# Performance work log

Hardware: AMD Instinct MI355X
Metric: run time of the kernel (lower is better)

## Reference

```python
import jax, jax.numpy as jnp
import numpy as np
import math

D_MODEL = 512
N_HEADS = 2
B, S = 2, 1024
THRESHOLD = 0.5  # kwargs default 'sparsity_threshold'


def setup_inputs() -> dict:
    key = jax.random.key(0)
    ks = jax.random.split(key, 10)
    D, H = D_MODEL, D_MODEL // 4
    std = 0.02
    return {
        "x": jax.random.normal(ks[0], (B, S, D), jnp.float32),
        "Wq": jax.random.normal(ks[1], (D, D), jnp.float32) * std,
        "Wk": jax.random.normal(ks[2], (D, D), jnp.float32) * std,
        "Wv": jax.random.normal(ks[3], (D, D), jnp.float32) * std,
        "Wo": jax.random.normal(ks[4], (D, D), jnp.float32) * std,
        "bo": jnp.zeros((D,), jnp.float32),
        "W1": jax.random.normal(ks[5], (D, H), jnp.float32) * std,
        "b1": jnp.zeros((H,), jnp.float32),
        "W2": jax.random.normal(ks[6], (H, 1), jnp.float32) * std,
        "b2": jnp.zeros((1,), jnp.float32),
    }


def reference(x, Wq, Wk, Wv, Wo, bo, W1, b1, W2, b2):
    Bsz, Seq, D = x.shape
    Hn = N_HEADS
    dh = D // Hn

    def split_heads(t):
        return t.reshape(Bsz, Seq, Hn, dh).transpose(0, 2, 1, 3)  # [B,H,S,dh]

    q = split_heads(x @ Wq)
    k = split_heads(x @ Wk)
    v = split_heads(x @ Wv)

    scores = jnp.einsum("bhid,bhjd->bhij", q, k) / math.sqrt(dh)  # [B,H,S,S]

    # head-mean features for the pairwise sparsity predictor (n_heads==2 => 2*dh == D)
    q_mean = q.mean(axis=1)  # [B,S,dh]
    k_mean = k.mean(axis=1)  # [B,S,dh]
    # Linear1 of cat([q_mean_i, k_mean_j]) splits into two halves of W1
    a = q_mean @ W1[:dh]   # [B,S,Dh4]
    c = k_mean @ W1[dh:]   # [B,S,Dh4]
    hidden = jax.nn.relu(a[:, :, None, :] + c[:, None, :, :] + b1)  # [B,S,S,Dh4]
    connection_probs = jax.nn.sigmoid(jnp.squeeze(hidden @ W2, -1) + b2[0])  # [B,S,S]

    mask = connection_probs > THRESHOLD  # [B,S,S]
    scores = jnp.where(mask[:, None, :, :], scores, jnp.float32(-1e9))
    attn = jax.nn.softmax(scores, axis=-1)  # dropout inactive in eval

    out = jnp.einsum("bhij,bhjd->bhid", attn, v)  # [B,H,S,dh]
    out = out.transpose(0, 2, 1, 3).reshape(Bsz, Seq, D)
    out = out @ Wo + bo
    return out
```

## Files before the change

### kernel.cpp

```cpp
#include <hip/hip_runtime.h>


typedef unsigned short u16t;
typedef __bf16 bf16x8 __attribute__((ext_vector_type(8)));
typedef float f32x4 __attribute__((ext_vector_type(4)));

#define B_SZ 2
#define S_SZ 1024
#define D_SZ 512
#define DH 256
#define HH 128

static __device__ __forceinline__ u16t f2b(float f) {
    unsigned int u = __builtin_bit_cast(unsigned int, f);
    u += 0x7FFFu + ((u >> 16) & 1u);
    return (u16t)(u >> 16);
}

static __device__ __forceinline__ f32x4 mfma16(bf16x8 a, bf16x8 b, f32x4 c) {
    return __builtin_amdgcn_mfma_f32_16x16x32_bf16(a, b, c, 0, 0, 0);
}

static __device__ __forceinline__ void gload16(const void* g, void* l) {
    __builtin_amdgcn_global_load_lds(
        (const __attribute__((address_space(1))) void*)g,
        (__attribute__((address_space(3))) void*)l, 16, 0, 0);
}

__global__ __launch_bounds__(256) void k_prep(
    const float* __restrict__ x,
    const float* __restrict__ Wq, const float* __restrict__ Wk,
    const float* __restrict__ Wv, const float* __restrict__ Wo,
    const float* __restrict__ W1,
    u16t* __restrict__ xb, u16t* __restrict__ WT, float* __restrict__ Beff)
{
    __shared__ float smf[1088];
    int bidx = blockIdx.x;
    int t = threadIdx.x;
    if (bidx < 1024) {
        int idx = (bidx * 256 + t) * 4;
        float4 v = *(const float4*)(x + idx);
        u16t* o = xb + idx;
        o[0] = f2b(v.x); o[1] = f2b(v.y); o[2] = f2b(v.z); o[3] = f2b(v.w);
    } else if (bidx < 2048) {
        int t2 = bidx - 1024;
        int z = t2 >> 8, rem = t2 & 255;
        int n0 = (rem & 15) * 32, k0 = (rem >> 4) * 32;
        const float* W = z == 0 ? Wq : z == 1 ? Wk : z == 2 ? Wv : Wo;
        u16t* WTz = WT + (size_t)z * D_SZ * D_SZ;
        float (*tile)[33] = (float(*)[33])smf;
        int r = t >> 3, c4 = (t & 7) * 4;
        float4 v = *(const float4*)(W + (size_t)(k0 + r) * D_SZ + n0 + c4);
        tile[r][c4] = v.x; tile[r][c4 + 1] = v.y; tile[r][c4 + 2] = v.z; tile[r][c4 + 3] = v.w;
        __syncthreads();
        u16t o[4];
        o[0] = f2b(tile[c4][r]); o[1] = f2b(tile[c4 + 1][r]);
        o[2] = f2b(tile[c4 + 2][r]); o[3] = f2b(tile[c4 + 3][r]);
        *(ushort4*)(WTz + (size_t)(n0 + r) * D_SZ + k0 + c4) = *(ushort4*)o;
    } else {
        int k = bidx - 2048;
        float* wm0 = smf;
        float* wm1 = smf + 256;
        const float* wrq = Wq + (size_t)k * D_SZ;
        const float* wrk = Wk + (size_t)k * D_SZ;
        wm0[t & 255] = 0.5f * (wrq[t & 255] + wrq[(t & 255) + DH]);
        wm1[t & 255] = 0.5f * (wrk[t & 255] + wrk[(t & 255) + DH]);
        __syncthreads();
        int half = t >> 7, hcol = t & 127;
        const float* wm = half ? wm1 : wm0;
        const float* W1h = W1 + (half ? (size_t)DH * HH : 0);
        float s = 0.f;
        for (int d = 0; d < 256; ++d) s += wm[d] * W1h[(size_t)d * HH + hcol];
        Beff[(size_t)k * 256 + half * 128 + hcol] = s;
    }
}

template<int NF>
static __device__ __forceinline__ void gemm_mainloop(
    const u16t* __restrict__ A, int lda, const u16t* __restrict__ B, int ldb,
    int K, int tid, u16t* Als, u16t* Bls, f32x4 acc[2][NF])
{
    const int w = tid >> 6, lane = tid & 63;
    const int lr = lane & 15, kg = lane >> 4;
    const int srow = lane >> 3, scol = (lane & 7) * 8;
    for (int k0 = 0; k0 < K; k0 += 64) {
        if (k0) __syncthreads();
#pragma unroll
        for (int q = 0; q < 4; ++q) {
            int ci = w * 4 + q;
            gload16(A + (size_t)(ci * 8 + srow) * lda + k0 + scol, Als + ci * 512);
        }
#pragma unroll
        for (int q = 0; q < NF / 2; ++q) {
            int cj = w * (NF / 2) + q;
            gload16(B + (size_t)(cj * 8 + srow) * ldb + k0 + scol, Bls + cj * 512);
        }
        __syncthreads();
#pragma unroll
        for (int kk = 0; kk < 2; ++kk) {
            bf16x8 af[2], bfr[NF];
#pragma unroll
            for (int fi = 0; fi < 2; ++fi)
                af[fi] = *(const bf16x8*)(&Als[(w * 32 + fi * 16 + lr) * 64 + kk * 32 + kg * 8]);
#pragma unroll
            for (int fj = 0; fj < NF; ++fj)
                bfr[fj] = *(const bf16x8*)(&Bls[(fj * 16 + lr) * 64 + kk * 32 + kg * 8]);
#pragma unroll
            for (int fi = 0; fi < 2; ++fi)
#pragma unroll
                for (int fj = 0; fj < NF; ++fj)
                    acc[fi][fj] = mfma16(af[fi], bfr[fj], acc[fi][fj]);
        }
    }
}


__global__ __launch_bounds__(256) void k_qkvac(
    const u16t* __restrict__ xb, const u16t* __restrict__ WT,
    const float* __restrict__ x, const float* __restrict__ Beff,
    const float* __restrict__ b1,
    u16t* __restrict__ qb, u16t* __restrict__ kb, u16t* __restrict__ vT,
    float* __restrict__ a, float* __restrict__ cc)
{
    __shared__ __align__(16) char sm[27648];
    int bid = blockIdx.x;
    int t = threadIdx.x;
    if (bid < 384) {
        u16t* Als = (u16t*)sm;
        u16t* Bls = Als + 8192;
        int z = bid / 128, rem = bid & 127;
        int m0 = (rem >> 3) * 128, n0 = (rem & 7) * 64;
        const u16t* A = xb + (size_t)m0 * D_SZ;
        const u16t* Bt = WT + (size_t)z * D_SZ * D_SZ + (size_t)n0 * D_SZ;
        f32x4 acc[2][4] = {};
        gemm_mainloop<4>(A, D_SZ, Bt, D_SZ, D_SZ, t, Als, Bls, acc);
        int w = t >> 6, lane = t & 63, lr = lane & 15, kg = lane >> 4;
        __syncthreads();
        if (z < 2) {
            u16t (*vls)[68] = (u16t(*)[68])sm;
            float scale = z == 0 ? 0.0625f : 1.0f;
#pragma unroll
            for (int fi = 0; fi < 2; ++fi)
#pragma unroll
                for (int fj = 0; fj < 4; ++fj)
#pragma unroll
                    for (int rr = 0; rr < 4; ++rr)
                        vls[w * 32 + fi * 16 + kg * 4 + rr][fj * 16 + lr]
                            = f2b(acc[fi][fj][rr] * scale);
            __syncthreads();
            u16t* dst = z == 0 ? qb : kb;
            int c8 = (t & 7) * 8, r0 = t >> 3;
#pragma unroll
            for (int p = 0; p < 4; ++p) {
                int r = r0 + p * 32;
                *(uint4*)(dst + (size_t)(m0 + r) * D_SZ + n0 + c8) = *(const uint4*)(&vls[r][c8]);
            }
        } else {
            u16t (*vls)[136] = (u16t(*)[136])sm;
#pragma unroll
            for (int fi = 0; fi < 2; ++fi)
#pragma unroll
                for (int fj = 0; fj < 4; ++fj)
#pragma unroll
                    for (int rr = 0; rr < 4; ++rr)
                        vls[fj * 16 + lr][w * 32 + fi * 16 + kg * 4 + rr] = f2b(acc[fi][fj][rr]);
            __syncthreads();
            int b = m0 >> 10, s0 = m0 & 1023;
            int cr = t >> 2, seg = t & 3;
            const u16t* srcp = &vls[cr][seg * 32];
            u16t* dstp = vT + (((size_t)(b * D_SZ + n0 + cr)) << 10) + s0 + seg * 32;
#pragma unroll
            for (int qq = 0; qq < 4; ++qq)
                *(uint4*)(dstp + qq * 8) = *(const uint4*)(srcp + qq * 8);
        }
    } else {
        float (*xs)[68] = (float(*)[68])sm;
        float (*bsT)[68] = (float(*)[68])(sm + 17408);
        int t2 = bid - 384;
        int r0 = (t2 & 31) * 64, n0 = (t2 >> 5) * 32;
        int ti = t >> 4, tj = t & 15;
        float acc[4][2] = {};
        for (int k0 = 0; k0 < 512; k0 += 64) {
            if (k0) __syncthreads();
#pragma unroll
            for (int p = 0; p < 4; ++p) {
                int idx = t + p * 256;
                int r = idx >> 4, c4 = (idx & 15) * 4;
                *(float4*)&xs[r][c4] = *(const float4*)(x + (size_t)(r0 + r) * D_SZ + k0 + c4);
            }
#pragma unroll
            for (int p = 0; p < 2; ++p) {
                int idx = t + p * 256;
                int k = idx >> 3, n4 = (idx & 7) * 4;
                float4 v = *(const float4*)(Beff + (size_t)(k0 + k) * 256 + n0 + n4);
                bsT[n4][k] = v.x; bsT[n4 + 1][k] = v.y; bsT[n4 + 2][k] = v.z; bsT[n4 + 3][k] = v.w;
            }
            __syncthreads();
#pragma unroll
            for (int kk = 0; kk < 16; ++kk) {
                float4 xv[4], bv[2];
#pragma unroll
                for (int ri = 0; ri < 4; ++ri) xv[ri] = *(const float4*)&xs[ti + 16 * ri][kk * 4];
#pragma unroll
                for (int rj = 0; rj < 2; ++rj) bv[rj] = *(const float4*)&bsT[tj + 16 * rj][kk * 4];
#pragma unroll
                for (int ri = 0; ri < 4; ++ri)
#pragma unroll
                    for (int rj = 0; rj < 2; ++rj)
                        acc[ri][rj] += xv[ri].x * bv[rj].x + xv[ri].y * bv[rj].y
                                     + xv[ri].z * bv[rj].z + xv[ri].w * bv[rj].w;
            }
        }
        bool isA = n0 < 128;
#pragma unroll
        for (int rj = 0; rj < 2; ++rj) {
            int col = n0 + tj + 16 * rj;
            float badd = isA ? b1[col] : 0.f;
#pragma unroll
            for (int ri = 0; ri < 4; ++ri) {
                int row = r0 + ti + 16 * ri;
                if (isA) a[(size_t)row * HH + col] = acc[ri][rj] + badd;
                else     cc[(size_t)row * HH + (col - 128)] = acc[ri][rj];
            }
        }
    }
}

__global__ __launch_bounds__(256) void k_mask(
    const float* __restrict__ a, const float* __restrict__ c,
    const float* __restrict__ W2, const float* __restrict__ b2,
    unsigned char* __restrict__ maskb)
{
    __shared__ __align__(16) float at[64][132];
    __shared__ __align__(16) float ct[64][132];
    __shared__ __align__(16) float w2s[128];
    int b = blockIdx.z, i0 = blockIdx.y * 64, j0 = blockIdx.x * 64;
    int t = threadIdx.x;
    if (t < 128) w2s[t] = W2[t];
#pragma unroll
    for (int p = 0; p < 8; ++p) {
        int idx = t + p * 256;
        int r = idx >> 5, c4 = (idx & 31) * 4;
        *(float4*)&at[r][c4] = *(const float4*)(a + ((size_t)(b * S_SZ + i0 + r)) * HH + c4);
        *(float4*)&ct[r][c4] = *(const float4*)(c + ((size_t)(b * S_SZ + j0 + r)) * HH + c4);
    }
    __syncthreads();
    float fb2 = b2[0];
    int ti = t >> 4, tj = t & 15;
    float acc[4][4];
#pragma unroll
    for (int ri = 0; ri < 4; ++ri)
#pragma unroll
        for (int rj = 0; rj < 4; ++rj) acc[ri][rj] = fb2;
#pragma unroll 2
    for (int h4 = 0; h4 < 32; ++h4) {
        float4 av[4], cv[4];
        float4 wv = ((const float4*)w2s)[h4];
#pragma unroll
        for (int ri = 0; ri < 4; ++ri) av[ri] = *(const float4*)&at[ti + 16 * ri][h4 * 4];
#pragma unroll
        for (int rj = 0; rj < 4; ++rj) cv[rj] = *(const float4*)&ct[tj + 16 * rj][h4 * 4];
#pragma unroll
        for (int ri = 0; ri < 4; ++ri)
#pragma unroll
            for (int rj = 0; rj < 4; ++rj) {
                acc[ri][rj] += fmaxf(av[ri].x + cv[rj].x, 0.f) * wv.x;
                acc[ri][rj] += fmaxf(av[ri].y + cv[rj].y, 0.f) * wv.y;
                acc[ri][rj] += fmaxf(av[ri].z + cv[rj].z, 0.f) * wv.z;
                acc[ri][rj] += fmaxf(av[ri].w + cv[rj].w, 0.f) * wv.w;
            }
    }
#pragma unroll
    for (int ri = 0; ri < 4; ++ri)
#pragma unroll
        for (int rj = 0; rj < 4; ++rj) {
            int i = i0 + ti + 16 * ri, j = j0 + tj + 16 * rj;
            maskb[((size_t)b << 20) + ((size_t)i << 10) + j] = acc[ri][rj] > 0.f ? 1 : 0;
        }
}

__global__ __launch_bounds__(256) void k_scores(
    const u16t* __restrict__ qb, const u16t* __restrict__ kb,
    const unsigned char* __restrict__ maskb, u16t* __restrict__ P,
    float* __restrict__ lpart)
{
    __shared__ __align__(16) u16t sm[12288];
    u16t* Als = sm;
    u16t* Bls = sm + 8192;
    int bh = blockIdx.z, b = bh >> 1, h = bh & 1;
    int jb = blockIdx.x;
    int m0 = blockIdx.y * 128, n0 = jb * 64;
    const u16t* A = qb + (size_t)b * S_SZ * D_SZ + (size_t)m0 * D_SZ + h * DH;
    const u16t* Bt = kb + (size_t)b * S_SZ * D_SZ + (size_t)n0 * D_SZ + h * DH;
    f32x4 acc[2][4] = {};
    gemm_mainloop<4>(A, D_SZ, Bt, D_SZ, DH, threadIdx.x, Als, Bls, acc);
    int w = threadIdx.x >> 6, lane = threadIdx.x & 63, lr = lane & 15, kg = lane >> 4;
#pragma unroll
    for (int fi = 0; fi < 2; ++fi)
#pragma unroll
        for (int rr = 0; rr < 4; ++rr) {
            int i = m0 + w * 32 + fi * 16 + kg * 4 + rr;
            float rs = 0.f;
#pragma unroll
            for (int fj = 0; fj < 4; ++fj) {
                int j = n0 + fj * 16 + lr;
                bool msk = maskb[((size_t)b << 20) + ((size_t)i << 10) + j] != 0;
                float e = msk ? __expf(acc[fi][fj][rr]) : 0.f;
                acc[fi][fj][rr] = e;
                rs += e;
            }
            rs += __shfl_xor(rs, 1); rs += __shfl_xor(rs, 2);
            rs += __shfl_xor(rs, 4); rs += __shfl_xor(rs, 8);
            if (lr == 0) lpart[((size_t)(jb * 4 + bh) << 10) + i] = rs;
        }
    __syncthreads();
    u16t (*vls)[68] = (u16t(*)[68])sm;
#pragma unroll
    for (int fi = 0; fi < 2; ++fi)
#pragma unroll
        for (int fj = 0; fj < 4; ++fj)
#pragma unroll
            for (int rr = 0; rr < 4; ++rr)
                vls[w * 32 + fi * 16 + kg * 4 + rr][fj * 16 + lr] = f2b(acc[fi][fj][rr]);
    __syncthreads();
    int c8 = (threadIdx.x & 7) * 8, r0 = threadIdx.x >> 3;
#pragma unroll
    for (int p = 0; p < 4; ++p) {
        int r = r0 + p * 32;
        *(uint4*)(P + ((size_t)bh << 20) + ((size_t)(m0 + r) << 10) + n0 + c8)
            = *(const uint4*)(&vls[r][c8]);
    }
}

__global__ __launch_bounds__(256) void k_pv(
    const u16t* __restrict__ P, const u16t* __restrict__ vT,
    const float* __restrict__ lpart, u16t* __restrict__ ao)
{
    __shared__ __align__(16) u16t sm[10240];
    __shared__ float invl[128];
    u16t* Als = sm;
    u16t* Bls = sm + 8192;
    int bh = blockIdx.z, b = bh >> 1, h = bh & 1;
    int m0 = blockIdx.y * 128, n0 = blockIdx.x * 32;
    int t = threadIdx.x;
    if (t < 128) {
        float l = 0.f;
        for (int jb = 0; jb < 16; ++jb)
            l += lpart[((size_t)(jb * 4 + bh) << 10) + m0 + t];
        invl[t] = l > 0.f ? 1.0f / l : 0.f;
    }
    const u16t* A = P + ((size_t)bh << 20) + (size_t)m0 * S_SZ;
    const u16t* Bt = vT + ((size_t)(b * D_SZ + h * DH + n0)) * S_SZ;
    f32x4 acc[2][2] = {};
    gemm_mainloop<2>(A, S_SZ, Bt, S_SZ, S_SZ, t, Als, Bls, acc);
    int w = t >> 6, lane = t & 63, lr = lane & 15, kg = lane >> 4;
    __syncthreads();
    u16t (*ols)[40] = (u16t(*)[40])sm;
#pragma unroll
    for (int fi = 0; fi < 2; ++fi) {
        int rl = w * 32 + fi * 16 + kg * 4;
#pragma unroll
        for (int fj = 0; fj < 2; ++fj)
#pragma unroll
            for (int rr = 0; rr < 4; ++rr)
                ols[rl + rr][fj * 16 + lr] = f2b(acc[fi][fj][rr] * invl[rl + rr]);
    }
    __syncthreads();
    int c8 = (t & 3) * 8, r0 = t >> 2;
#pragma unroll
    for (int p = 0; p < 2; ++p) {
        int r = r0 + p * 64;
        *(uint4*)(ao + ((size_t)(b * S_SZ + m0 + r)) * D_SZ + h * DH + n0 + c8)
            = *(const uint4*)(&ols[r][c8]);
    }
}

__global__ __launch_bounds__(256) void k_out(
    const u16t* __restrict__ ao, const u16t* __restrict__ WoT,
    const float* __restrict__ bo, float* __restrict__ out)
{
    __shared__ __align__(16) u16t sm[10240];
    u16t* Als = sm;
    u16t* Bls = sm + 8192;
    int m0 = blockIdx.y * 128, n0 = blockIdx.x * 32;
    const u16t* A = ao + (size_t)m0 * D_SZ;
    const u16t* Bt = WoT + (size_t)n0 * D_SZ;
    f32x4 acc[2][2] = {};
    gemm_mainloop<2>(A, D_SZ, Bt, D_SZ, D_SZ, threadIdx.x, Als, Bls, acc);
    int w = threadIdx.x >> 6, lane = threadIdx.x & 63, lr = lane & 15, kg = lane >> 4;
    __syncthreads();
    float (*ols)[36] = (float(*)[36])sm;
#pragma unroll
    for (int fi = 0; fi < 2; ++fi)
#pragma unroll
        for (int fj = 0; fj < 2; ++fj)
#pragma unroll
            for (int rr = 0; rr < 4; ++rr) {
                int rl = w * 32 + fi * 16 + kg * 4 + rr;
                ols[rl][fj * 16 + lr] = acc[fi][fj][rr] + bo[n0 + fj * 16 + lr];
            }
    __syncthreads();
    int c4 = (threadIdx.x & 7) * 4, r0 = threadIdx.x >> 3;
#pragma unroll
    for (int p = 0; p < 4; ++p) {
        int r = r0 + p * 32;
        *(float4*)(out + (size_t)(m0 + r) * D_SZ + n0 + c4) = *(const float4*)(&ols[r][c4]);
    }
}

extern "C" void kernel_launch(void* const* d_in, const int* in_sizes, int n_in,
                              void* d_out, int out_size, void* d_ws, size_t ws_size,
                              hipStream_t stream)
{
    const float* x  = (const float*)d_in[0];
    const float* Wq = (const float*)d_in[1];
    const float* Wk = (const float*)d_in[2];
    const float* Wv = (const float*)d_in[3];
    const float* Wo = (const float*)d_in[4];
    const float* bo = (const float*)d_in[5];
    const float* W1 = (const float*)d_in[6];
    const float* b1 = (const float*)d_in[7];
    const float* W2 = (const float*)d_in[8];
    const float* b2 = (const float*)d_in[9];
    float* out = (float*)d_out;

    char* ws = (char*)d_ws;
    size_t off = 0;
    auto carve = [&](size_t bytes) { void* p = ws + off; off += (bytes + 255) & ~(size_t)255; return p; };
    u16t* xb   = (u16t*)carve((size_t)2048 * 512 * 2);
    u16t* WT   = (u16t*)carve((size_t)4 * 512 * 512 * 2);
    u16t* qb   = (u16t*)carve((size_t)2048 * 512 * 2);
    u16t* kb   = (u16t*)carve((size_t)2048 * 512 * 2);
    u16t* vT   = (u16t*)carve((size_t)2 * 512 * 1024 * 2);
    float* Beff = (float*)carve((size_t)512 * 256 * 4);
    float* a   = (float*)carve((size_t)2048 * 128 * 4);
    float* c   = (float*)carve((size_t)2048 * 128 * 4);
    unsigned char* maskb = (unsigned char*)carve((size_t)2 * 1024 * 1024);
    u16t* P    = (u16t*)carve((size_t)4 * 1024 * 1024 * 2);
    float* lpart = (float*)carve((size_t)16 * 4 * 1024 * 4);
    u16t* ao   = (u16t*)carve((size_t)2048 * 512 * 2);
    (void)ws_size;

    k_prep<<<dim3(2560), dim3(256), 0, stream>>>(x, Wq, Wk, Wv, Wo, W1, xb, WT, Beff);
    k_qkvac<<<dim3(640), dim3(256), 0, stream>>>(xb, WT, x, Beff, b1, qb, kb, vT, a, c);
    k_mask<<<dim3(16, 16, 2), dim3(256), 0, stream>>>(a, c, W2, b2, maskb);
    k_scores<<<dim3(16, 8, 4), dim3(256), 0, stream>>>(qb, kb, maskb, P, lpart);
    k_pv<<<dim3(8, 8, 4), dim3(256), 0, stream>>>(P, vT, lpart, ao);
    k_out<<<dim3(16, 16), dim3(256), 0, stream>>>(ao, WT + (size_t)3 * 512 * 512, bo, out);
}
```

Baseline: 110.2 us.

## Compute predictor projections with split-bf16 MFMA and fuse mask into QKV launch

The fp32 scalar GEMM that produced the predictor features a/c is replaced by a dedicated kernel using bf16 MFMA with a hi/lo split (three products per tile) to keep near-fp32 accuracy. The pairwise mask computation moves out of its own launch and runs as extra blocks of the QKV projection kernel, with its LDS footprint cut by chunking the hidden dimension. This removes scalar FMA cost and overlaps mask work with the QKV GEMM. In exchange it adds a kernel that must finish before QKV, an extra low-part copy of x, and some risk of mask flips near the threshold from reduced precision.

Result: slower. 115.0 us (+4.4%).

```diff
diff --git a/kernel.cpp b/kernel.cpp
--- a/kernel.cpp
+++ b/kernel.cpp
@@ -16,6 +16,9 @@
     u += 0x7FFFu + ((u >> 16) & 1u);
     return (u16t)(u >> 16);
 }
+static __device__ __forceinline__ float b2f(u16t u) {
+    return __builtin_bit_cast(float, (unsigned int)u << 16);
+}
 
 static __device__ __forceinline__ f32x4 mfma16(bf16x8 a, bf16x8 b, f32x4 c) {
     return __builtin_amdgcn_mfma_f32_16x16x32_bf16(a, b, c, 0, 0, 0);
@@ -32,7 +35,8 @@
     const float* __restrict__ Wq, const float* __restrict__ Wk,
     const float* __restrict__ Wv, const float* __restrict__ Wo,
     const float* __restrict__ W1,
-    u16t* __restrict__ xb, u16t* __restrict__ WT, float* __restrict__ Beff)
+    u16t* __restrict__ xb, u16t* __restrict__ xl,
+    u16t* __restrict__ WT, float* __restrict__ Beff)
 {
     __shared__ float smf[1088];
     int bidx = blockIdx.x;
@@ -40,8 +44,12 @@
     if (bidx < 1024) {
         int idx = (bidx * 256 + t) * 4;
         float4 v = *(const float4*)(x + idx);
-        u16t* o = xb + idx;
-        o[0] = f2b(v.x); o[1] = f2b(v.y); o[2] = f2b(v.z); o[3] = f2b(v.w);
+        u16t h[4], l[4];
+        h[0] = f2b(v.x); h[1] = f2b(v.y); h[2] = f2b(v.z); h[3] = f2b(v.w);
+        l[0] = f2b(v.x - b2f(h[0])); l[1] = f2b(v.y - b2f(h[1]));
+        l[2] = f2b(v.z - b2f(h[2])); l[3] = f2b(v.w - b2f(h[3]));
+        *(ushort4*)(xb + idx) = *(ushort4*)h;
+        *(ushort4*)(xl + idx) = *(ushort4*)l;
     } else if (bidx < 2048) {
         int t2 = bidx - 1024;
         int z = t2 >> 8, rem = t2 & 255;
@@ -115,14 +123,87 @@
 }
 
 
-__global__ __launch_bounds__(256) void k_qkvac(
+__global__ __launch_bounds__(256) void k_ac(
+    const u16t* __restrict__ xb, const u16t* __restrict__ xl,
+    const float* __restrict__ Beff, const float* __restrict__ b1,
+    float* __restrict__ a, float* __restrict__ cc)
+{
+    __shared__ u16t Ah[128 * 64];
+    __shared__ u16t Alo[128 * 64];
+    __shared__ u16t Bh[32 * 72];
+    __shared__ u16t Bl[32 * 72];
+    int m0 = blockIdx.x * 128, n0 = blockIdx.y * 32;
+    int t = threadIdx.x;
+    const int w = t >> 6, lane = t & 63, lr = lane & 15, kg = lane >> 4;
+    const int srow = lane >> 3, scol = (lane & 7) * 8;
+    f32x4 acc[2][2] = {};
+    for (int k0 = 0; k0 < 512; k0 += 64) {
+        if (k0) __syncthreads();
+#pragma unroll
+        for (int q = 0; q < 4; ++q) {
+            int ci = w * 4 + q;
+            gload16(xb + (size_t)(m0 + ci * 8 + srow) * D_SZ + k0 + scol, Ah + ci * 512);
+            gload16(xl + (size_t)(m0 + ci * 8 + srow) * D_SZ + k0 + scol, Alo + ci * 512);
+        }
+        {
+            int nn = t & 31, kq = t >> 5;
+#pragma unroll
+            for (int p = 0; p < 8; ++p) {
+                int k = kq + p * 8;
+                float v = Beff[(size_t)(k0 + k) * 256 + n0 + nn];
+                u16t hi = f2b(v);
+                Bh[nn * 72 + k] = hi;
+                Bl[nn * 72 + k] = f2b(v - b2f(hi));
+            }
+        }
+        __syncthreads();
+#pragma unroll
+        for (int kk = 0; kk < 2; ++kk) {
+            bf16x8 ah[2], al2[2], bh[2], bl2[2];
+#pragma unroll
+            for (int fi = 0; fi < 2; ++fi) {
+                ah[fi]  = *(const bf16x8*)(&Ah [(w * 32 + fi * 16 + lr) * 64 + kk * 32 + kg * 8]);
+                al2[fi] = *(const bf16x8*)(&Alo[(w * 32 + fi * 16 + lr) * 64 + kk * 32 + kg * 8]);
+            }
+#pragma unroll
+            for (int fj = 0; fj < 2; ++fj) {
+                bh[fj]  = *(const bf16x8*)(&Bh[(fj * 16 + lr) * 72 + kk * 32 + kg * 8]);
+                bl2[fj] = *(const bf16x8*)(&Bl[(fj * 16 + lr) * 72 + kk * 32 + kg * 8]);
+            }
+#pragma unroll
+            for (int fi = 0; fi < 2; ++fi)
+#pragma unroll
+                for (int fj = 0; fj < 2; ++fj) {
+                    acc[fi][fj] = mfma16(ah[fi],  bh[fj],  acc[fi][fj]);
+                    acc[fi][fj] = mfma16(ah[fi],  bl2[fj], acc[fi][fj]);
+                    acc[fi][fj] = mfma16(al2[fi], bh[fj],  acc[fi][fj]);
+                }
+        }
+    }
+    bool isA = n0 < 128;
+#pragma unroll
+    for (int fi = 0; fi < 2; ++fi)
+#pragma unroll
+        for (int fj = 0; fj < 2; ++fj) {
+            int col = n0 + fj * 16 + lr;
+            float badd = isA ? b1[col] : 0.f;
+#pragma unroll
+            for (int rr = 0; rr < 4; ++rr) {
+                int row = m0 + w * 32 + fi * 16 + kg * 4 + rr;
+                if (isA) a[(size_t)row * HH + col] = acc[fi][fj][rr] + badd;
+                else     cc[(size_t)row * HH + (col - 128)] = acc[fi][fj][rr];
+            }
+        }
+}
+
+__global__ __launch_bounds__(256) void k_qkvmask(
     const u16t* __restrict__ xb, const u16t* __restrict__ WT,
-    const float* __restrict__ x, const float* __restrict__ Beff,
-    const float* __restrict__ b1,
+    const float* __restrict__ a, const float* __restrict__ c,
+    const float* __restrict__ W2, const float* __restrict__ b2,
     u16t* __restrict__ qb, u16t* __restrict__ kb, u16t* __restrict__ vT,
-    float* __restrict__ a, float* __restrict__ cc)
-{
-    __shared__ __align__(16) char sm[27648];
+    unsigned char* __restrict__ maskb)
+{
+    __shared__ __align__(16) char sm[24576];
     int bid = blockIdx.x;
     int t = threadIdx.x;
     if (bid < 384) {
@@ -174,109 +255,57 @@
                 *(uint4*)(dstp + qq * 8) = *(const uint4*)(srcp + qq * 8);
         }
     } else {
-        float (*xs)[68] = (float(*)[68])sm;
-        float (*bsT)[68] = (float(*)[68])(sm + 17408);
+        float (*at)[36] = (float(*)[36])sm;
+        float (*ct)[36] = (float(*)[36])(sm + 9216);
+        float* w2s = (float*)(sm + 18432);
         int t2 = bid - 384;
-        int r0 = (t2 & 31) * 64, n0 = (t2 >> 5) * 32;
+        int b = t2 >> 8, rem = t2 & 255;
+        int i0 = (rem >> 4) * 64, j0 = (rem & 15) * 64;
+        if (t < 128) w2s[t] = W2[t];
+        float fb2 = b2[0];
         int ti = t >> 4, tj = t & 15;
-        float acc[4][2] = {};
-        for (int k0 = 0; k0 < 512; k0 += 64) {
-            if (k0) __syncthreads();
-#pragma unroll
-            for (int p = 0; p < 4; ++p) {
-                int idx = t + p * 256;
-                int r = idx >> 4, c4 = (idx & 15) * 4;
-                *(float4*)&xs[r][c4] = *(const float4*)(x + (size_t)(r0 + r) * D_SZ + k0 + c4);
-            }
-#pragma unroll
-            for (int p = 0; p < 2; ++p) {
-                int idx = t + p * 256;
-                int k = idx >> 3, n4 = (idx & 7) * 4;
-                float4 v = *(const float4*)(Beff + (size_t)(k0 + k) * 256 + n0 + n4);
-                bsT[n4][k] = v.x; bsT[n4 + 1][k] = v.y; bsT[n4 + 2][k] = v.z; bsT[n4 + 3][k] = v.w;
-            }
+        float acc[4][4];
+#pragma unroll
+        for (int ri = 0; ri < 4; ++ri)
+#pragma unroll
+            for (int rj = 0; rj < 4; ++rj) acc[ri][rj] = fb2;
+        int sr = t >> 2, sc = (t & 3) * 8;
+        for (int hc = 0; hc < 4; ++hc) {
             __syncthreads();
-#pragma unroll
-            for (int kk = 0; kk < 16; ++kk) {
-                float4 xv[4], bv[2];
-#pragma unroll
-                for (int ri = 0; ri < 4; ++ri) xv[ri] = *(const float4*)&xs[ti + 16 * ri][kk * 4];
-#pragma unroll
-                for (int rj = 0; rj < 2; ++rj) bv[rj] = *(const float4*)&bsT[tj + 16 * rj][kk * 4];
+            const float* ap = a + (size_t)(b * S_SZ + i0 + sr) * HH + hc * 32 + sc;
+            const float* cp = c + (size_t)(b * S_SZ + j0 + sr) * HH + hc * 32 + sc;
+            *(float4*)&at[sr][sc]     = *(const float4*)ap;
+            *(float4*)&at[sr][sc + 4] = *(const float4*)(ap + 4);
+            *(float4*)&ct[sr][sc]     = *(const float4*)cp;
+            *(float4*)&ct[sr][sc + 4] = *(const float4*)(cp + 4);
+            __syncthreads();
+#pragma unroll
+            for (int h4 = 0; h4 < 8; ++h4) {
+                float4 wv = *(const float4*)&w2s[hc * 32 + h4 * 4];
+                float4 av[4], cv[4];
+#pragma unroll
+                for (int ri = 0; ri < 4; ++ri) av[ri] = *(const float4*)&at[ti + 16 * ri][h4 * 4];
+#pragma unroll
+                for (int rj = 0; rj < 4; ++rj) cv[rj] = *(const float4*)&ct[tj + 16 * rj][h4 * 4];
 #pragma unroll
                 for (int ri = 0; ri < 4; ++ri)
 #pragma unroll
-                    for (int rj = 0; rj < 2; ++rj)
-                        acc[ri][rj] += xv[ri].x * bv[rj].x + xv[ri].y * bv[rj].y
-                                     + xv[ri].z * bv[rj].z + xv[ri].w * bv[rj].w;
-            }
-        }
-        bool isA = n0 < 128;
-#pragma unroll
-        for (int rj = 0; rj < 2; ++rj) {
-            int col = n0 + tj + 16 * rj;
-            float badd = isA ? b1[col] : 0.f;
-#pragma unroll
-            for (int ri = 0; ri < 4; ++ri) {
-                int row = r0 + ti + 16 * ri;
-                if (isA) a[(size_t)row * HH + col] = acc[ri][rj] + badd;
-                else     cc[(size_t)row * HH + (col - 128)] = acc[ri][rj];
-            }
-        }
-    }
-}
-
-__global__ __launch_bounds__(256) void k_mask(
-    const float* __restrict__ a, const float* __restrict__ c,
-    const float* __restrict__ W2, const float* __restrict__ b2,
-    unsigned char* __restrict__ maskb)
-{
-    __shared__ __align__(16) float at[64][132];
-    __shared__ __align__(16) float ct[64][132];
-    __shared__ __align__(16) float w2s[128];
-    int b = blockIdx.z, i0 = blockIdx.y * 64, j0 = blockIdx.x * 64;
-    int t = threadIdx.x;
-    if (t < 128) w2s[t] = W2[t];
-#pragma unroll
-    for (int p = 0; p < 8; ++p) {
-        int idx = t + p * 256;
-        int r = idx >> 5, c4 = (idx & 31) * 4;
-        *(float4*)&at[r][c4] = *(const float4*)(a + ((size_t)(b * S_SZ + i0 + r)) * HH + c4);
-        *(float4*)&ct[r][c4] = *(const float4*)(c + ((size_t)(b * S_SZ + j0 + r)) * HH + c4);
-    }
-    __syncthreads();
-    float fb2 = b2[0];
-    int ti = t >> 4, tj = t & 15;
-    float acc[4][4];
-#pragma unroll
-    for (int ri = 0; ri < 4; ++ri)
-#pragma unroll
-        for (int rj = 0; rj < 4; ++rj) acc[ri][rj] = fb2;
-#pragma unroll 2
-    for (int h4 = 0; h4 < 32; ++h4) {
-        float4 av[4], cv[4];
-        float4 wv = ((const float4*)w2s)[h4];
-#pragma unroll
-        for (int ri = 0; ri < 4; ++ri) av[ri] = *(const float4*)&at[ti + 16 * ri][h4 * 4];
-#pragma unroll
-        for (int rj = 0; rj < 4; ++rj) cv[rj] = *(const float4*)&ct[tj + 16 * rj][h4 * 4];
+                    for (int rj = 0; rj < 4; ++rj) {
+                        acc[ri][rj] += fmaxf(av[ri].x + cv[rj].x, 0.f) * wv.x;
+                        acc[ri][rj] += fmaxf(av[ri].y + cv[rj].y, 0.f) * wv.y;
+                        acc[ri][rj] += fmaxf(av[ri].z + cv[rj].z, 0.f) * wv.z;
+                        acc[ri][rj] += fmaxf(av[ri].w + cv[rj].w, 0.f) * wv.w;
+                    }
+            }
+        }
 #pragma unroll
         for (int ri = 0; ri < 4; ++ri)
 #pragma unroll
             for (int rj = 0; rj < 4; ++rj) {
-                acc[ri][rj] += fmaxf(av[ri].x + cv[rj].x, 0.f) * wv.x;
-                acc[ri][rj] += fmaxf(av[ri].y + cv[rj].y, 0.f) * wv.y;
-                acc[ri][rj] += fmaxf(av[ri].z + cv[rj].z, 0.f) * wv.z;
-                acc[ri][rj] += fmaxf(av[ri].w + cv[rj].w, 0.f) * wv.w;
-            }
-    }
-#pragma unroll
-    for (int ri = 0; ri < 4; ++ri)
-#pragma unroll
-        for (int rj = 0; rj < 4; ++rj) {
-            int i = i0 + ti + 16 * ri, j = j0 + tj + 16 * rj;
-            maskb[((size_t)b << 20) + ((size_t)i << 10) + j] = acc[ri][rj] > 0.f ? 1 : 0;
-        }
+                int i = i0 + ti + 16 * ri, j = j0 + tj + 16 * rj;
+                maskb[((size_t)b << 20) + ((size_t)i << 10) + j] = acc[ri][rj] > 0.f ? 1 : 0;
+            }
+    }
 }
 
 __global__ __launch_bounds__(256) void k_scores(
@@ -428,6 +457,7 @@
     size_t off = 0;
     auto carve = [&](size_t bytes) { void* p = ws + off; off += (bytes + 255) & ~(size_t)255; return p; };
     u16t* xb   = (u16t*)carve((size_t)2048 * 512 * 2);
+    u16t* xl   = (u16t*)carve((size_t)2048 * 512 * 2);
     u16t* WT   = (u16t*)carve((size_t)4 * 512 * 512 * 2);
     u16t* qb   = (u16t*)carve((size_t)2048 * 512 * 2);
     u16t* kb   = (u16t*)carve((size_t)2048 * 512 * 2);
@@ -441,9 +471,9 @@
     u16t* ao   = (u16t*)carve((size_t)2048 * 512 * 2);
     (void)ws_size;
 
-    k_prep<<<dim3(2560), dim3(256), 0, stream>>>(x, Wq, Wk, Wv, Wo, W1, xb, WT, Beff);
-    k_qkvac<<<dim3(640), dim3(256), 0, stream>>>(xb, WT, x, Beff, b1, qb, kb, vT, a, c);
-    k_mask<<<dim3(16, 16, 2), dim3(256), 0, stream>>>(a, c, W2, b2, maskb);
+    k_prep<<<dim3(2560), dim3(256), 0, stream>>>(x, Wq, Wk, Wv, Wo, W1, xb, xl, WT, Beff);
+    k_ac<<<dim3(16, 8), dim3(256), 0, stream>>>(xb, xl, Beff, b1, a, c);
+    k_qkvmask<<<dim3(896), dim3(256), 0, stream>>>(xb, WT, a, c, W2, b2, qb, kb, vT, maskb);
     k_scores<<<dim3(16, 8, 4), dim3(256), 0, stream>>>(qb, kb, maskb, P, lpart);
     k_pv<<<dim3(8, 8, 4), dim3(256), 0, stream>>>(P, vT, lpart, ao);
     k_out<<<dim3(16, 16), dim3(256), 0, stream>>>(ao, WT + (size_t)3 * 512 * 512, bo, out);
```

## Replace LDS-staged GEMM mainloop with direct global-to-register MFMA fragment loads

Applied to the files above, without the earlier changes.

Swaps the shared GEMM mainloop, which staged A/B tiles into LDS via global_load_lds with two barriers per K step, for a fully unrolled loop in which each wave loads its bf16x8 MFMA fragments straight from global memory. All four GEMM kernels (QKV, scores, PV, output projection) use the new path, their shared-memory footprints shrink, and barriers before the epilogues are removed. The goal is to cut LDS traffic and synchronisation, at the cost of losing cross-wave reuse of the B tile: every wave now fetches the same B fragments through cache, and the scattered 16-byte row loads may be less coalesced.

New measurement: 122.2 us. 10.9% more time.

```diff
diff --git a/kernel.cpp b/kernel.cpp
--- a/kernel.cpp
+++ b/kernel.cpp
@@ -16,15 +16,12 @@
     u += 0x7FFFu + ((u >> 16) & 1u);
     return (u16t)(u >> 16);
 }
+static __device__ __forceinline__ float b2f(u16t u) {
+    return __builtin_bit_cast(float, (unsigned int)u << 16);
+}
 
 static __device__ __forceinline__ f32x4 mfma16(bf16x8 a, bf16x8 b, f32x4 c) {
     return __builtin_amdgcn_mfma_f32_16x16x32_bf16(a, b, c, 0, 0, 0);
-}
-
-static __device__ __forceinline__ void gload16(const void* g, void* l) {
-    __builtin_amdgcn_global_load_lds(
-        (const __attribute__((address_space(1))) void*)g,
-        (__attribute__((address_space(3))) void*)l, 16, 0, 0);
 }
 
 __global__ __launch_bounds__(256) void k_prep(
@@ -75,42 +72,29 @@
     }
 }
 
-template<int NF>
-static __device__ __forceinline__ void gemm_mainloop(
+template<int NF, int K>
+static __device__ __forceinline__ void gemm_direct(
     const u16t* __restrict__ A, int lda, const u16t* __restrict__ B, int ldb,
-    int K, int tid, u16t* Als, u16t* Bls, f32x4 acc[2][NF])
+    int tid, f32x4 acc[2][NF])
 {
     const int w = tid >> 6, lane = tid & 63;
     const int lr = lane & 15, kg = lane >> 4;
-    const int srow = lane >> 3, scol = (lane & 7) * 8;
-    for (int k0 = 0; k0 < K; k0 += 64) {
-        if (k0) __syncthreads();
-#pragma unroll
-        for (int q = 0; q < 4; ++q) {
-            int ci = w * 4 + q;
-            gload16(A + (size_t)(ci * 8 + srow) * lda + k0 + scol, Als + ci * 512);
-        }
-#pragma unroll
-        for (int q = 0; q < NF / 2; ++q) {
-            int cj = w * (NF / 2) + q;
-            gload16(B + (size_t)(cj * 8 + srow) * ldb + k0 + scol, Bls + cj * 512);
-        }
-        __syncthreads();
-#pragma unroll
-        for (int kk = 0; kk < 2; ++kk) {
-            bf16x8 af[2], bfr[NF];
-#pragma unroll
-            for (int fi = 0; fi < 2; ++fi)
-                af[fi] = *(const bf16x8*)(&Als[(w * 32 + fi * 16 + lr) * 64 + kk * 32 + kg * 8]);
+    const u16t* Ap = A + (size_t)(w * 32 + lr) * lda + kg * 8;
+    const u16t* Bp = B + (size_t)lr * ldb + kg * 8;
+#pragma unroll
+    for (int k0 = 0; k0 < K; k0 += 32) {
+        bf16x8 af[2], bfr[NF];
+#pragma unroll
+        for (int fi = 0; fi < 2; ++fi)
+            af[fi] = *(const bf16x8*)(Ap + (size_t)fi * 16 * lda + k0);
+#pragma unroll
+        for (int fj = 0; fj < NF; ++fj)
+            bfr[fj] = *(const bf16x8*)(Bp + (size_t)fj * 16 * ldb + k0);
+#pragma unroll
+        for (int fi = 0; fi < 2; ++fi)
 #pragma unroll
             for (int fj = 0; fj < NF; ++fj)
-                bfr[fj] = *(const bf16x8*)(&Bls[(fj * 16 + lr) * 64 + kk * 32 + kg * 8]);
-#pragma unroll
-            for (int fi = 0; fi < 2; ++fi)
-#pragma unroll
-                for (int fj = 0; fj < NF; ++fj)
-                    acc[fi][fj] = mfma16(af[fi], bfr[fj], acc[fi][fj]);
-        }
+                acc[fi][fj] = mfma16(af[fi], bfr[fj], acc[fi][fj]);
     }
 }
 
@@ -126,16 +110,13 @@
     int bid = blockIdx.x;
     int t = threadIdx.x;
     if (bid < 384) {
-        u16t* Als = (u16t*)sm;
-        u16t* Bls = Als + 8192;
         int z = bid / 128, rem = bid & 127;
         int m0 = (rem >> 3) * 128, n0 = (rem & 7) * 64;
         const u16t* A = xb + (size_t)m0 * D_SZ;
         const u16t* Bt = WT + (size_t)z * D_SZ * D_SZ + (size_t)n0 * D_SZ;
         f32x4 acc[2][4] = {};
-        gemm_mainloop<4>(A, D_SZ, Bt, D_SZ, D_SZ, t, Als, Bls, acc);
+        gemm_direct<4, 512>(A, D_SZ, Bt, D_SZ, t, acc);
         int w = t >> 6, lane = t & 63, lr = lane & 15, kg = lane >> 4;
-        __syncthreads();
         if (z < 2) {
             u16t (*vls)[68] = (u16t(*)[68])sm;
             float scale = z == 0 ? 0.0625f : 1.0f;
@@ -284,16 +265,14 @@
     const unsigned char* __restrict__ maskb, u16t* __restrict__ P,
     float* __restrict__ lpart)
 {
-    __shared__ __align__(16) u16t sm[12288];
-    u16t* Als = sm;
-    u16t* Bls = sm + 8192;
+    __shared__ __align__(16) u16t sm[128 * 68];
     int bh = blockIdx.z, b = bh >> 1, h = bh & 1;
     int jb = blockIdx.x;
     int m0 = blockIdx.y * 128, n0 = jb * 64;
     const u16t* A = qb + (size_t)b * S_SZ * D_SZ + (size_t)m0 * D_SZ + h * DH;
     const u16t* Bt = kb + (size_t)b * S_SZ * D_SZ + (size_t)n0 * D_SZ + h * DH;
     f32x4 acc[2][4] = {};
-    gemm_mainloop<4>(A, D_SZ, Bt, D_SZ, DH, threadIdx.x, Als, Bls, acc);
+    gemm_direct<4, 256>(A, D_SZ, Bt, D_SZ, threadIdx.x, acc);
     int w = threadIdx.x >> 6, lane = threadIdx.x & 63, lr = lane & 15, kg = lane >> 4;
 #pragma unroll
     for (int fi = 0; fi < 2; ++fi)
@@ -313,7 +292,6 @@
             rs += __shfl_xor(rs, 4); rs += __shfl_xor(rs, 8);
             if (lr == 0) lpart[((size_t)(jb * 4 + bh) << 10) + i] = rs;
         }
-    __syncthreads();
     u16t (*vls)[68] = (u16t(*)[68])sm;
 #pragma unroll
     for (int fi = 0; fi < 2; ++fi)
@@ -336,10 +314,8 @@
     const u16t* __restrict__ P, const u16t* __restrict__ vT,
     const float* __restrict__ lpart, u16t* __restrict__ ao)
 {
-    __shared__ __align__(16) u16t sm[10240];
+    __shared__ __align__(16) u16t sm[128 * 40];
     __shared__ float invl[128];
-    u16t* Als = sm;
-    u16t* Bls = sm + 8192;
     int bh = blockIdx.z, b = bh >> 1, h = bh & 1;
     int m0 = blockIdx.y * 128, n0 = blockIdx.x * 32;
     int t = threadIdx.x;
@@ -349,12 +325,12 @@
             l += lpart[((size_t)(jb * 4 + bh) << 10) + m0 + t];
         invl[t] = l > 0.f ? 1.0f / l : 0.f;
     }
+    __syncthreads();
     const u16t* A = P + ((size_t)bh << 20) + (size_t)m0 * S_SZ;
     const u16t* Bt = vT + ((size_t)(b * D_SZ + h * DH + n0)) * S_SZ;
     f32x4 acc[2][2] = {};
-    gemm_mainloop<2>(A, S_SZ, Bt, S_SZ, S_SZ, t, Als, Bls, acc);
+    gemm_direct<2, 1024>(A, S_SZ, Bt, S_SZ, t, acc);
     int w = t >> 6, lane = t & 63, lr = lane & 15, kg = lane >> 4;
-    __syncthreads();
     u16t (*ols)[40] = (u16t(*)[40])sm;
 #pragma unroll
     for (int fi = 0; fi < 2; ++fi) {
@@ -379,17 +355,13 @@
     const u16t* __restrict__ ao, const u16t* __restrict__ WoT,
     const float* __restrict__ bo, float* __restrict__ out)
 {
-    __shared__ __align__(16) u16t sm[10240];
-    u16t* Als = sm;
-    u16t* Bls = sm + 8192;
+    __shared__ __align__(16) float ols[128][36];
     int m0 = blockIdx.y * 128, n0 = blockIdx.x * 32;
     const u16t* A = ao + (size_t)m0 * D_SZ;
     const u16t* Bt = WoT + (size_t)n0 * D_SZ;
     f32x4 acc[2][2] = {};
-    gemm_mainloop<2>(A, D_SZ, Bt, D_SZ, D_SZ, threadIdx.x, Als, Bls, acc);
+    gemm_direct<2, 512>(A, D_SZ, Bt, D_SZ, threadIdx.x, acc);
     int w = threadIdx.x >> 6, lane = threadIdx.x & 63, lr = lane & 15, kg = lane >> 4;
-    __syncthreads();
-    float (*ols)[36] = (float(*)[36])sm;
 #pragma unroll
     for (int fi = 0; fi < 2; ++fi)
 #pragma unroll
```

## Double-buffer GEMM mainloop and halve M tiles for scores, PV and output

Applied to the files above, without the earlier changes.

Replaces the single-buffered GEMM mainloop with a double-buffered version that issues the next K-tile's global-to-LDS loads before computing on the current one, so each iteration needs one barrier instead of two. The scores, PV and output-projection kernels also drop from 128-row to 64-row M tiles, doubling their grid sizes to fill more CUs. The cost is twice the LDS per block and less per-block reuse of the B operand, plus rewritten epilogue indexing for the smaller tiles.

Result: faster. 104.8 us (-4.8%).

```diff
diff --git a/kernel.cpp b/kernel.cpp
--- a/kernel.cpp
+++ b/kernel.cpp
@@ -75,42 +75,54 @@
     }
 }
 
-template<int NF>
-static __device__ __forceinline__ void gemm_mainloop(
+template<int MF, int NF>
+static __device__ __forceinline__ void gemm_db(
     const u16t* __restrict__ A, int lda, const u16t* __restrict__ B, int ldb,
-    int K, int tid, u16t* Als, u16t* Bls, f32x4 acc[2][NF])
+    int K, int tid, u16t* Als, u16t* Bls, f32x4 acc[MF][NF])
 {
     const int w = tid >> 6, lane = tid & 63;
     const int lr = lane & 15, kg = lane >> 4;
     const int srow = lane >> 3, scol = (lane & 7) * 8;
-    for (int k0 = 0; k0 < K; k0 += 64) {
-        if (k0) __syncthreads();
-#pragma unroll
-        for (int q = 0; q < 4; ++q) {
-            int ci = w * 4 + q;
-            gload16(A + (size_t)(ci * 8 + srow) * lda + k0 + scol, Als + ci * 512);
+    const int ABUF = MF * 4096;
+    const int BBUF = NF * 1024;
+    auto stage = [&](int bb, int k0) {
+#pragma unroll
+        for (int q = 0; q < MF * 2; ++q) {
+            int ci = w * (MF * 2) + q;
+            gload16(A + (size_t)(ci * 8 + srow) * lda + k0 + scol,
+                    Als + bb * ABUF + ci * 512);
         }
 #pragma unroll
         for (int q = 0; q < NF / 2; ++q) {
             int cj = w * (NF / 2) + q;
-            gload16(B + (size_t)(cj * 8 + srow) * ldb + k0 + scol, Bls + cj * 512);
-        }
-        __syncthreads();
+            gload16(B + (size_t)(cj * 8 + srow) * ldb + k0 + scol,
+                    Bls + bb * BBUF + cj * 512);
+        }
+    };
+    stage(0, 0);
+    __syncthreads();
+    const int nt = K / 64;
+    for (int t = 0; t < nt; ++t) {
+        int cur = t & 1;
+        if (t + 1 < nt) stage(cur ^ 1, (t + 1) * 64);
+        const u16t* Ab = Als + cur * ABUF;
+        const u16t* Bb = Bls + cur * BBUF;
 #pragma unroll
         for (int kk = 0; kk < 2; ++kk) {
-            bf16x8 af[2], bfr[NF];
-#pragma unroll
-            for (int fi = 0; fi < 2; ++fi)
-                af[fi] = *(const bf16x8*)(&Als[(w * 32 + fi * 16 + lr) * 64 + kk * 32 + kg * 8]);
+            bf16x8 af[MF], bfr[NF];
+#pragma unroll
+            for (int fi = 0; fi < MF; ++fi)
+                af[fi] = *(const bf16x8*)(&Ab[(w * (MF * 16) + fi * 16 + lr) * 64 + kk * 32 + kg * 8]);
 #pragma unroll
             for (int fj = 0; fj < NF; ++fj)
-                bfr[fj] = *(const bf16x8*)(&Bls[(fj * 16 + lr) * 64 + kk * 32 + kg * 8]);
-#pragma unroll
-            for (int fi = 0; fi < 2; ++fi)
+                bfr[fj] = *(const bf16x8*)(&Bb[(fj * 16 + lr) * 64 + kk * 32 + kg * 8]);
+#pragma unroll
+            for (int fi = 0; fi < MF; ++fi)
 #pragma unroll
                 for (int fj = 0; fj < NF; ++fj)
                     acc[fi][fj] = mfma16(af[fi], bfr[fj], acc[fi][fj]);
         }
+        __syncthreads();
     }
 }
 
@@ -122,20 +134,19 @@
     u16t* __restrict__ qb, u16t* __restrict__ kb, u16t* __restrict__ vT,
     float* __restrict__ a, float* __restrict__ cc)
 {
-    __shared__ __align__(16) char sm[27648];
+    __shared__ __align__(16) char sm[49152];
     int bid = blockIdx.x;
     int t = threadIdx.x;
     if (bid < 384) {
         u16t* Als = (u16t*)sm;
-        u16t* Bls = Als + 8192;
+        u16t* Bls = (u16t*)(sm + 32768);
         int z = bid / 128, rem = bid & 127;
         int m0 = (rem >> 3) * 128, n0 = (rem & 7) * 64;
         const u16t* A = xb + (size_t)m0 * D_SZ;
         const u16t* Bt = WT + (size_t)z * D_SZ * D_SZ + (size_t)n0 * D_SZ;
         f32x4 acc[2][4] = {};
-        gemm_mainloop<4>(A, D_SZ, Bt, D_SZ, D_SZ, t, Als, Bls, acc);
+        gemm_db<2, 4>(A, D_SZ, Bt, D_SZ, D_SZ, t, Als, Bls, acc);
         int w = t >> 6, lane = t & 63, lr = lane & 15, kg = lane >> 4;
-        __syncthreads();
         if (z < 2) {
             u16t (*vls)[68] = (u16t(*)[68])sm;
             float scale = z == 0 ? 0.0625f : 1.0f;
@@ -284,66 +295,59 @@
     const unsigned char* __restrict__ maskb, u16t* __restrict__ P,
     float* __restrict__ lpart)
 {
-    __shared__ __align__(16) u16t sm[12288];
+    __shared__ __align__(16) u16t sm[16384];
     u16t* Als = sm;
     u16t* Bls = sm + 8192;
     int bh = blockIdx.z, b = bh >> 1, h = bh & 1;
     int jb = blockIdx.x;
-    int m0 = blockIdx.y * 128, n0 = jb * 64;
+    int m0 = blockIdx.y * 64, n0 = jb * 64;
     const u16t* A = qb + (size_t)b * S_SZ * D_SZ + (size_t)m0 * D_SZ + h * DH;
     const u16t* Bt = kb + (size_t)b * S_SZ * D_SZ + (size_t)n0 * D_SZ + h * DH;
-    f32x4 acc[2][4] = {};
-    gemm_mainloop<4>(A, D_SZ, Bt, D_SZ, DH, threadIdx.x, Als, Bls, acc);
+    f32x4 acc[1][4] = {};
+    gemm_db<1, 4>(A, D_SZ, Bt, D_SZ, DH, threadIdx.x, Als, Bls, acc);
     int w = threadIdx.x >> 6, lane = threadIdx.x & 63, lr = lane & 15, kg = lane >> 4;
 #pragma unroll
-    for (int fi = 0; fi < 2; ++fi)
-#pragma unroll
-        for (int rr = 0; rr < 4; ++rr) {
-            int i = m0 + w * 32 + fi * 16 + kg * 4 + rr;
-            float rs = 0.f;
-#pragma unroll
-            for (int fj = 0; fj < 4; ++fj) {
-                int j = n0 + fj * 16 + lr;
-                bool msk = maskb[((size_t)b << 20) + ((size_t)i << 10) + j] != 0;
-                float e = msk ? __expf(acc[fi][fj][rr]) : 0.f;
-                acc[fi][fj][rr] = e;
-                rs += e;
-            }
-            rs += __shfl_xor(rs, 1); rs += __shfl_xor(rs, 2);
-            rs += __shfl_xor(rs, 4); rs += __shfl_xor(rs, 8);
-            if (lr == 0) lpart[((size_t)(jb * 4 + bh) << 10) + i] = rs;
-        }
+    for (int rr = 0; rr < 4; ++rr) {
+        int i = m0 + w * 16 + kg * 4 + rr;
+        float rs = 0.f;
+#pragma unroll
+        for (int fj = 0; fj < 4; ++fj) {
+            int j = n0 + fj * 16 + lr;
+            bool msk = maskb[((size_t)b << 20) + ((size_t)i << 10) + j] != 0;
+            float e = msk ? __expf(acc[0][fj][rr]) : 0.f;
+            acc[0][fj][rr] = e;
+            rs += e;
+        }
+        rs += __shfl_xor(rs, 1); rs += __shfl_xor(rs, 2);
+        rs += __shfl_xor(rs, 4); rs += __shfl_xor(rs, 8);
+        if (lr == 0) lpart[((size_t)(jb * 4 + bh) << 10) + i] = rs;
+    }
     __syncthreads();
     u16t (*vls)[68] = (u16t(*)[68])sm;
 #pragma unroll
-    for (int fi = 0; fi < 2; ++fi)
-#pragma unroll
-        for (int fj = 0; fj < 4; ++fj)
-#pragma unroll
-            for (int rr = 0; rr < 4; ++rr)
-                vls[w * 32 + fi * 16 + kg * 4 + rr][fj * 16 + lr] = f2b(acc[fi][fj][rr]);
-    __syncthreads();
-    int c8 = (threadIdx.x & 7) * 8, r0 = threadIdx.x >> 3;
-#pragma unroll
-    for (int p = 0; p < 4; ++p) {
-        int r = r0 + p * 32;
-        *(uint4*)(P + ((size_t)bh << 20) + ((size_t)(m0 + r) << 10) + n0 + c8)
-            = *(const uint4*)(&vls[r][c8]);
-    }
+    for (int fj = 0; fj < 4; ++fj)
+#pragma unroll
+        for (int rr = 0; rr < 4; ++rr)
+            vls[w * 16 + kg * 4 + rr][fj * 16 + lr] = f2b(acc[0][fj][rr]);
+    __syncthreads();
+    int r = threadIdx.x >> 2, c16 = (threadIdx.x & 3) * 16;
+    u16t* dstp = P + ((size_t)bh << 20) + ((size_t)(m0 + r) << 10) + n0 + c16;
+    *(uint4*)dstp = *(const uint4*)(&vls[r][c16]);
+    *(uint4*)(dstp + 8) = *(const uint4*)(&vls[r][c16 + 8]);
 }
 
 __global__ __launch_bounds__(256) void k_pv(
     const u16t* __restrict__ P, const u16t* __restrict__ vT,
     const float* __restrict__ lpart, u16t* __restrict__ ao)
 {
-    __shared__ __align__(16) u16t sm[10240];
-    __shared__ float invl[128];
+    __shared__ __align__(16) u16t sm[12288];
+    __shared__ float invl[64];
     u16t* Als = sm;
     u16t* Bls = sm + 8192;
     int bh = blockIdx.z, b = bh >> 1, h = bh & 1;
-    int m0 = blockIdx.y * 128, n0 = blockIdx.x * 32;
+    int m0 = blockIdx.y * 64, n0 = blockIdx.x * 32;
     int t = threadIdx.x;
-    if (t < 128) {
+    if (t < 64) {
         float l = 0.f;
         for (int jb = 0; jb < 16; ++jb)
             l += lpart[((size_t)(jb * 4 + bh) << 10) + m0 + t];
@@ -351,58 +355,48 @@
     }
     const u16t* A = P + ((size_t)bh << 20) + (size_t)m0 * S_SZ;
     const u16t* Bt = vT + ((size_t)(b * D_SZ + h * DH + n0)) * S_SZ;
-    f32x4 acc[2][2] = {};
-    gemm_mainloop<2>(A, S_SZ, Bt, S_SZ, S_SZ, t, Als, Bls, acc);
+    f32x4 acc[1][2] = {};
+    gemm_db<1, 2>(A, S_SZ, Bt, S_SZ, S_SZ, t, Als, Bls, acc);
     int w = t >> 6, lane = t & 63, lr = lane & 15, kg = lane >> 4;
-    __syncthreads();
     u16t (*ols)[40] = (u16t(*)[40])sm;
 #pragma unroll
-    for (int fi = 0; fi < 2; ++fi) {
-        int rl = w * 32 + fi * 16 + kg * 4;
-#pragma unroll
-        for (int fj = 0; fj < 2; ++fj)
-#pragma unroll
-            for (int rr = 0; rr < 4; ++rr)
-                ols[rl + rr][fj * 16 + lr] = f2b(acc[fi][fj][rr] * invl[rl + rr]);
-    }
-    __syncthreads();
-    int c8 = (t & 3) * 8, r0 = t >> 2;
-#pragma unroll
-    for (int p = 0; p < 2; ++p) {
-        int r = r0 + p * 64;
-        *(uint4*)(ao + ((size_t)(b * S_SZ + m0 + r)) * D_SZ + h * DH + n0 + c8)
-            = *(const uint4*)(&ols[r][c8]);
-    }
+    for (int fj = 0; fj < 2; ++fj)
+#pragma unroll
+        for (int rr = 0; rr < 4; ++rr) {
+            int rl = w * 16 + kg * 4 + rr;
+            ols[rl][fj * 16 + lr] = f2b(acc[0][fj][rr] * invl[rl]);
+        }
+    __syncthreads();
+    int r = t >> 2, c8 = (t & 3) * 8;
+    *(uint4*)(ao + ((size_t)(b * S_SZ + m0 + r)) * D_SZ + h * DH + n0 + c8)
+        = *(const uint4*)(&ols[r][c8]);
 }
 
 __global__ __launch_bounds__(256) void k_out(
     const u16t* __restrict__ ao, const u16t* __restrict__ WoT,
     const float* __restrict__ bo, float* __restrict__ out)
 {
-    __shared__ __align__(16) u16t sm[10240];
+    __shared__ __align__(16) u16t sm[12288];
     u16t* Als = sm;
     u16t* Bls = sm + 8192;
-    int m0 = blockIdx.y * 128, n0 = blockIdx.x * 32;
+    int m0 = blockIdx.y * 64, n0 = blockIdx.x * 32;
     const u16t* A = ao + (size_t)m0 * D_SZ;
     const u16t* Bt = WoT + (size_t)n0 * D_SZ;
-    f32x4 acc[2][2] = {};
-    gemm_mainloop<2>(A, D_SZ, Bt, D_SZ, D_SZ, threadIdx.x, Als, Bls, acc);
+    f32x4 acc[1][2] = {};
+    gemm_db<1, 2>(A, D_SZ, Bt, D_SZ, D_SZ, threadIdx.x, Als, Bls, acc);
     int w = threadIdx.x >> 6, lane = threadIdx.x & 63, lr = lane & 15, kg = lane >> 4;
-    __syncthreads();
     float (*ols)[36] = (float(*)[36])sm;
 #pragma unroll
-    for (int fi = 0; fi < 2; ++fi)
-#pragma unroll
-        for (int fj = 0; fj < 2; ++fj)
-#pragma unroll
-            for (int rr = 0; rr < 4; ++rr) {
-                int rl = w * 32 + fi * 16 + kg * 4 + rr;
-                ols[rl][fj * 16 + lr] = acc[fi][fj][rr] + bo[n0 + fj * 16 + lr];
-            }
-    __syncthreads();
-    int c4 = (threadIdx.x & 7) * 4, r0 = threadIdx.x >> 3;
-#pragma unroll
-    for (int p = 0; p < 4; ++p) {
+    for (int fj = 0; fj < 2; ++fj)
+#pragma unroll
+        for (int rr = 0; rr < 4; ++rr) {
+            int rl = w * 16 + kg * 4 + rr;
+            ols[rl][fj * 16 + lr] = acc[0][fj][rr] + bo[n0 + fj * 16 + lr];
+        }
+    __syncthreads();
+    int r0 = threadIdx.x >> 3, c4 = (threadIdx.x & 7) * 4;
+#pragma unroll
+    for (int p = 0; p < 2; ++p) {
         int r = r0 + p * 32;
         *(float4*)(out + (size_t)(m0 + r) * D_SZ + n0 + c4) = *(const float4*)(&ols[r][c4]);
     }
@@ -444,7 +438,7 @@
     k_prep<<<dim3(2560), dim3(256), 0, stream>>>(x, Wq, Wk, Wv, Wo, W1, xb, WT, Beff);
     k_qkvac<<<dim3(640), dim3(256), 0, stream>>>(xb, WT, x, Beff, b1, qb, kb, vT, a, c);
     k_mask<<<dim3(16, 16, 2), dim3(256), 0, stream>>>(a, c, W2, b2, maskb);
-    k_scores<<<dim3(16, 8, 4), dim3(256), 0, stream>>>(qb, kb, maskb, P, lpart);
-    k_pv<<<dim3(8, 8, 4), dim3(256), 0, stream>>>(P, vT, lpart, ao);
-    k_out<<<dim3(16, 16), dim3(256), 0, stream>>>(ao, WT + (size_t)3 * 512 * 512, bo, out);
-}
+    k_scores<<<dim3(16, 16, 4), dim3(256), 0, stream>>>(qb, kb, maskb, P, lpart);
+    k_pv<<<dim3(8, 16, 4), dim3(256), 0, stream>>>(P, vT, lpart, ao);
+    k_out<<<dim3(16, 32), dim3(256), 0, stream>>>(ao, WT + (size_t)3 * 512 * 512, bo, out);
+}
```
